# Kernel optimization log

Measured on AMD Instinct MI355X. Metric: run time of the kernel, lower is better.

## Reference

```python
import jax, jax.numpy as jnp
import numpy as np

EPS = 1e-5
K = 3

def _bn(x, g, b):
    # training-mode BatchNorm2d: batch stats over (N,H,W), biased variance
    m = jnp.mean(x, axis=(0, 2, 3), keepdims=True)
    v = jnp.var(x, axis=(0, 2, 3), keepdims=True)
    return (x - m) * jax.lax.rsqrt(v + EPS) * g[None, :, None, None] + b[None, :, None, None]

def _gelu(x):
    return jax.nn.gelu(x, approximate=False)

def _dyn_dw(x, aw1, ab1, aw2, ab2):
    # dynamic depthwise conv: per-sample k^2 softmax weights shared over channels
    b, c, h, w = x.shape
    gap = jnp.mean(x, axis=(2, 3))                              # (b,c)
    h1 = jax.nn.relu(jnp.einsum('oc,bc->bo', aw1, gap) + ab1)   # (b,c//8)
    kw = jax.nn.softmax(jnp.einsum('oc,bc->bo', aw2, h1) + ab2, axis=1)  # (b,k^2)
    xp = jnp.pad(x, ((0, 0), (0, 0), (1, 1), (1, 1)))
    out = jnp.zeros_like(x)
    idx = 0
    for i in range(K):
        for j in range(K):
            out = out + kw[:, idx, None, None, None] * xp[:, :, i:i + h, j:j + w]
            idx += 1
    return out

def _channel_att(x, w1, w2):
    avg = jnp.mean(x, axis=(2, 3))        # (b,C)
    mx = jnp.max(x, axis=(2, 3))          # (b,C)
    def fc(v):
        return jnp.einsum('oc,bc->bo', w2, jax.nn.relu(jnp.einsum('oc,bc->bo', w1, v)))
    s = jax.nn.sigmoid(fc(avg) + fc(mx))  # (b,C)
    return s[:, :, None, None] * x

def _forward(x, w1, b1, g1, be1, aw1, ab1, aw2, ab2, g2, be2,
             ca_w1, ca_w2, pw, pb, g3, be3, sw, sb):
    b, n, d = x.shape
    h = w = int(np.sqrt(n))
    residual = x
    xi = jnp.transpose(x.reshape(b, h, w, d), (0, 3, 1, 2))       # (b,d,h,w)
    # pw_expand: 1x1 conv -> GELU -> BN
    y = jnp.einsum('oc,bchw->bohw', w1, xi) + b1[None, :, None, None]
    y = _bn(_gelu(y), g1, be1)                                    # (b,4d,h,w)
    # dw_conv: dynamic depthwise -> GELU -> BN -> channel attention
    y = _dyn_dw(y, aw1, ab1, aw2, ab2)
    y = _bn(_gelu(y), g2, be2)
    y = _channel_att(y, ca_w1, ca_w2)
    # spatial attention
    avg_o = jnp.mean(y, axis=1, keepdims=True)
    max_o = jnp.max(y, axis=1, keepdims=True)
    sp_in = jnp.concatenate([avg_o, max_o], axis=1)               # (b,2,h,w)
    sp = jax.lax.conv_general_dilated(sp_in, sw, (1, 1), ((3, 3), (3, 3)),
                                      dimension_numbers=('NCHW', 'OIHW', 'NCHW'))
    sp = jax.nn.sigmoid(sp + sb[None, :, None, None])
    y = y * sp
    # pw_project: 1x1 conv -> BN
    y = jnp.einsum('oc,bchw->bohw', pw, y) + pb[None, :, None, None]
    y = _bn(y, g3, be3)
    y = jnp.transpose(y, (0, 2, 3, 1)).reshape(b, n, d)
    return residual + y

def setup_inputs() -> dict:
    key = jax.random.key(0)
    ks = jax.random.split(key, 16)
    d, C = 256, 1024
    def rn(k, shape, fan):
        return jax.random.normal(k, shape, jnp.float32) * np.float32(np.sqrt(2.0 / fan))
    return {
        'x': jax.random.normal(ks[0], (8, 1024, d), jnp.float32),
        'w1': rn(ks[1], (C, d), d), 'b1': jnp.zeros((C,), jnp.float32),
        'g1': jnp.ones((C,), jnp.float32), 'be1': jnp.zeros((C,), jnp.float32),
        'aw1': rn(ks[2], (C // 8, C), C), 'ab1': jnp.zeros((C // 8,), jnp.float32),
        'aw2': rn(ks[3], (K * K, C // 8), C // 8), 'ab2': jnp.zeros((K * K,), jnp.float32),
        'g2': jnp.ones((C,), jnp.float32), 'be2': jnp.zeros((C,), jnp.float32),
        'ca_w1': rn(ks[4], (C // 16, C), C), 'ca_w2': rn(ks[5], (C, C // 16), C // 16),
        'pw': rn(ks[6], (d, C), C), 'pb': jnp.zeros((d,), jnp.float32),
        'g3': jnp.ones((d,), jnp.float32), 'be3': jnp.zeros((d,), jnp.float32),
        'sw': rn(ks[7], (1, 2, 7, 7), 2 * 49), 'sb': jnp.zeros((1,), jnp.float32),
    }

def reference(x, w1, b1, g1, be1, aw1, ab1, aw2, ab2, g2, be2,
              ca_w1, ca_w2, pw, pb, g3, be3, sw, sb):
    return _forward(x, w1, b1, g1, be1, aw1, ab1, aw2, ab2, g2, be2,
                    ca_w1, ca_w2, pw, pb, g3, be3, sw, sb)
```

## Files before the change

### kernel.cpp

```cpp
#include <hip/hip_runtime.h>
#include <math.h>

constexpr int B = 8;
constexpr int D = 256;
constexpr int C = 1024;
constexpr int H = 32, W = 32;
constexpr int P = H * W;
constexpr int M = B * P;
constexpr float EPS = 1e-5f;

typedef unsigned short u16;
typedef unsigned int u32;
typedef __attribute__((ext_vector_type(8))) short short8;
typedef __attribute__((ext_vector_type(4))) float floatx4;

constexpr size_t WS_CHSUM1 = 0;
constexpr size_t WS_CHSQ1  = 1024;
constexpr size_t WS_GAPSUM = 2048;
constexpr size_t WS_CHSUM3 = 10240;
constexpr size_t WS_CHSQ3  = 10496;
constexpr size_t WS_CHSUM2 = 10752;
constexpr size_t WS_CHSQ2  = 11776;
constexpr size_t WS_BSUM2  = 12800;
constexpr size_t WS_UMAX2  = 20992;
constexpr size_t WS_UMAXN2 = 29184;
constexpr size_t WS_ACC_COUNT = 37376;
constexpr size_t WS_SCALE1 = 37376;
constexpr size_t WS_SHIFT1 = 38400;
constexpr size_t WS_KW     = 39424;
constexpr size_t WS_SCALE2 = 39680;
constexpr size_t WS_SHIFT2 = 40704;
constexpr size_t WS_SATT   = 41728;
constexpr size_t WS_AVGO   = 49920;
constexpr size_t WS_MAXO   = 58112;
constexpr size_t WS_SP     = 66304;
constexpr size_t WS_PRE    = 74496;
constexpr size_t WS_T1B    = 2171648;
constexpr size_t WS_T2B    = 6365952;
constexpr size_t WS_XB     = 10560256;
constexpr size_t WS_W1B    = 11608832;
constexpr size_t WS_PWB    = 11739904;
constexpr size_t WS_YB     = 11870976;

__device__ __forceinline__ float gelu_exact(float v) {
    return 0.5f * v * (1.0f + erff(v * 0.70710678118654752440f));
}

__device__ __forceinline__ u16 f2bf(float f) {
    u32 u = __float_as_uint(f);
    u += 0x7fff + ((u >> 16) & 1);
    return (u16)(u >> 16);
}

__device__ __forceinline__ float bf2f(u16 v) {
    return __uint_as_float(((u32)v) << 16);
}

__device__ __forceinline__ u32 fkey(float f) {
    u32 u = __float_as_uint(f);
    return (u & 0x80000000u) ? ~u : (u | 0x80000000u);
}
__device__ __forceinline__ float fkeyinv(u32 k) {
    return __uint_as_float((k & 0x80000000u) ? (k ^ 0x80000000u) : ~k);
}

__global__ __launch_bounds__(256) void cvt_all_kernel(const float* __restrict__ x,
                                                      const float* __restrict__ w1,
                                                      const float* __restrict__ pw,
                                                      u16* __restrict__ xb,
                                                      u16* __restrict__ w1b,
                                                      u16* __restrict__ pwb,
                                                      float* __restrict__ acc_zero) {
    const int i = blockIdx.x * 256 + threadIdx.x;
    if (i < (int)WS_ACC_COUNT) acc_zero[i] = 0.f;
    const float* src;
    u16* dst;
    int off;
    if (i < 524288)      { src = x;  dst = xb;  off = i; }
    else if (i < 589824) { src = w1; dst = w1b; off = i - 524288; }
    else                 { src = pw; dst = pwb; off = i - 589824; }
    const float4 v = *(const float4*)(src + (size_t)off * 4);
    uint2 o;
    o.x = ((u32)f2bf(v.x)) | ((u32)f2bf(v.y) << 16);
    o.y = ((u32)f2bf(v.z)) | ((u32)f2bf(v.w) << 16);
    *(uint2*)(dst + (size_t)off * 4) = o;
}

template<int KD, int EPI, int NS, int MB, int NB>
__global__ __launch_bounds__(256) void mfma_gemm_kernel(
    const u16* __restrict__ A,
    const u16* __restrict__ Bw,
    const float* __restrict__ bias,
    const float* __restrict__ rowscale,
    void* __restrict__ outv,
    float* __restrict__ csum,
    float* __restrict__ csq,
    float* __restrict__ gsum)
{
    constexpr int MI = MB / 32;
    constexpr int NJ = NB / 32;
    constexpr int ASZ = MB * 32;
    constexpr int BSZ = NB * 32;
    extern __shared__ u16 smem[];
    u16* As0 = smem;
    u16* As1 = smem + ASZ;
    u16* Bs0 = smem + 2 * ASZ;
    u16* Bs1 = smem + 2 * ASZ + BSZ;
    const int t = threadIdx.x;
    const int lane = t & 63;
    const int row0 = blockIdx.y * MB;
    const int col0 = blockIdx.x * NB;
    const int wv = t >> 6;
    const int wrow = (wv >> 1) * (MB / 2);
    const int wcol = (wv & 1) * (NB / 2);
    const int lm = lane & 15;
    const int lk8 = (lane >> 4) * 8;
    const int srow = t >> 2;
    const int scol = (t & 3) * 8;
    const u16* gA0 = A + (size_t)(row0 + srow) * KD + scol;
    const u16* gA1 = A + (size_t)(row0 + 64 + srow) * KD + scol;
    const u16* gB0 = Bw + (size_t)(col0 + srow) * KD + scol;
    const floatx4 zero = {0.f, 0.f, 0.f, 0.f};
    floatx4 acc[MI][NJ];
#pragma unroll
    for (int i = 0; i < MI; ++i)
#pragma unroll
        for (int j = 0; j < NJ; ++j) acc[i][j] = zero;

    for (int k0 = 0; k0 < KD; k0 += 64) {
        __builtin_amdgcn_global_load_lds(
            (const __attribute__((address_space(1))) void*)(gA0 + k0),
            (__attribute__((address_space(3))) void*)(As0 + t * 8), 16, 0, 0);
        if (MB == 128)
            __builtin_amdgcn_global_load_lds(
                (const __attribute__((address_space(1))) void*)(gA1 + k0),
                (__attribute__((address_space(3))) void*)(As0 + 2048 + t * 8), 16, 0, 0);
        __builtin_amdgcn_global_load_lds(
            (const __attribute__((address_space(1))) void*)(gB0 + k0),
            (__attribute__((address_space(3))) void*)(Bs0 + t * 8), 16, 0, 0);
        __builtin_amdgcn_global_load_lds(
            (const __attribute__((address_space(1))) void*)(gA0 + k0 + 32),
            (__attribute__((address_space(3))) void*)(As1 + t * 8), 16, 0, 0);
        if (MB == 128)
            __builtin_amdgcn_global_load_lds(
                (const __attribute__((address_space(1))) void*)(gA1 + k0 + 32),
                (__attribute__((address_space(3))) void*)(As1 + 2048 + t * 8), 16, 0, 0);
        __builtin_amdgcn_global_load_lds(
            (const __attribute__((address_space(1))) void*)(gB0 + k0 + 32),
            (__attribute__((address_space(3))) void*)(Bs1 + t * 8), 16, 0, 0);
        __syncthreads();
#pragma unroll
        for (int buf = 0; buf < 2; ++buf) {
            const u16* As = buf ? As1 : As0;
            const u16* Bs = buf ? Bs1 : Bs0;
            short8 af[MI], bf[NJ];
#pragma unroll
            for (int i = 0; i < MI; ++i)
                af[i] = *(const short8*)(As + (wrow + i * 16 + lm) * 32 + lk8);
#pragma unroll
            for (int j = 0; j < NJ; ++j)
                bf[j] = *(const short8*)(Bs + (wcol + j * 16 + lm) * 32 + lk8);
#pragma unroll
            for (int i = 0; i < MI; ++i)
#pragma unroll
                for (int j = 0; j < NJ; ++j)
                    acc[i][j] = __builtin_amdgcn_mfma_f32_16x16x32_bf16(af[i], bf[j], acc[i][j], 0, 0, 0);
        }
        __syncthreads();
    }

    float colsum[NJ], colsq[NJ];
#pragma unroll
    for (int j = 0; j < NJ; ++j) { colsum[j] = 0.f; colsq[j] = 0.f; }

    if (EPI == 0) {
        u16* Cs = smem;
#pragma unroll
        for (int i = 0; i < MI; ++i) {
#pragma unroll
            for (int r = 0; r < 4; ++r) {
                const int lrow = wrow + i * 16 + (lane >> 4) * 4 + r;
#pragma unroll
                for (int j = 0; j < NJ; ++j) {
                    const int lcol = wcol + j * 16 + lm;
                    const float tv = gelu_exact(acc[i][j][r] + bias[col0 + lcol]);
                    Cs[lrow * NB + lcol] = f2bf(tv);
                    colsum[j] += tv;
                    colsq[j] = fmaf(tv, tv, colsq[j]);
                }
            }
        }
        __syncthreads();
        const int rr = t >> 1;
        const int hh = (t & 1) * 32;
        u16* outp = (u16*)outv + (size_t)(row0 + rr) * NS + col0 + hh;
#pragma unroll
        for (int k = 0; k < 4; ++k) {
            *(uint4*)(outp + k * 8) = *(const uint4*)(Cs + rr * NB + hh + k * 8);
        }
    } else {
        float* Cs = (float*)smem;
#pragma unroll
        for (int i = 0; i < MI; ++i) {
#pragma unroll
            for (int r = 0; r < 4; ++r) {
                const int lrow = wrow + i * 16 + (lane >> 4) * 4 + r;
                const float rs = rowscale[row0 + lrow];
#pragma unroll
                for (int j = 0; j < NJ; ++j) {
                    const int lcol = wcol + j * 16 + lm;
                    const float tv = rs * acc[i][j][r] + bias[col0 + lcol];
                    Cs[lrow * NB + lcol] = tv;
                    colsum[j] += tv;
                    colsq[j] = fmaf(tv, tv, colsq[j]);
                }
            }
        }
        __syncthreads();
        const int rr = t >> 2;
        const int hh = (t & 3) * 16;
        float* outp = (float*)outv + (size_t)(row0 + rr) * NS + col0 + hh;
#pragma unroll
        for (int k = 0; k < 4; ++k)
            *(float4*)(outp + k * 4) = *(const float4*)(Cs + rr * NB + hh + k * 4);
    }

    const int bb = (blockIdx.y * MB) >> 10;
#pragma unroll
    for (int j = 0; j < NJ; ++j) {
        float s = colsum[j];
        float q = colsq[j];
        s += __shfl_xor(s, 16); s += __shfl_xor(s, 32);
        q += __shfl_xor(q, 16); q += __shfl_xor(q, 32);
        if (lane < 16) {
            const int c = col0 + wcol + j * 16 + lm;
            atomicAdd(&csum[c], s);
            atomicAdd(&csq[c], q);
            if (EPI == 0) atomicAdd(&gsum[bb * NS + c], s);
        }
    }
}

__global__ __launch_bounds__(1024) void dynmlp_kernel(const float* __restrict__ chsum1,
                                                      const float* __restrict__ chsq1,
                                                      const float* __restrict__ gapsum,
                                                      const float* __restrict__ g1,
                                                      const float* __restrict__ be1,
                                                      const float* __restrict__ aw1,
                                                      const float* __restrict__ ab1,
                                                      const float* __restrict__ aw2,
                                                      const float* __restrict__ ab2,
                                                      float* __restrict__ scale1,
                                                      float* __restrict__ shift1,
                                                      float* __restrict__ kw) {
    const int b = blockIdx.x;
    const int t = threadIdx.x;
    const int wave = t >> 6, lane = t & 63;
    __shared__ float g[1024];
    __shared__ float h1[128];
    __shared__ float logits[12];
    {
        const float m = chsum1[t] * (1.0f / (float)M);
        const float var = chsq1[t] * (1.0f / (float)M) - m * m;
        const float rstd = rsqrtf(var + EPS);
        const float sc = rstd * g1[t];
        const float sh = be1[t] - m * sc;
        if (b == 0) { scale1[t] = sc; shift1[t] = sh; }
        g[t] = gapsum[b * C + t] * (1.0f / (float)P) * sc + sh;
    }
    __syncthreads();
#pragma unroll
    for (int k = 0; k < 8; ++k) {
        const int u = wave * 8 + k;
        const float4* wr = (const float4*)(aw1 + (size_t)u * C);
        float s = 0.f;
#pragma unroll
        for (int ch = 0; ch < 4; ++ch) {
            const float4 wv = wr[lane + 64 * ch];
            const float4 sv = *(const float4*)(g + 4 * lane + 256 * ch);
            s += wv.x * sv.x + wv.y * sv.y + wv.z * sv.z + wv.w * sv.w;
        }
#pragma unroll
        for (int off = 1; off < 64; off <<= 1) s += __shfl_xor(s, off);
        if (lane == 0) h1[u] = fmaxf(s + ab1[u], 0.f);
    }
    __syncthreads();
    if (wave < 9) {
        float s = aw2[wave * 128 + lane] * h1[lane]
                + aw2[wave * 128 + 64 + lane] * h1[64 + lane];
#pragma unroll
        for (int off = 1; off < 64; off <<= 1) s += __shfl_xor(s, off);
        if (lane == 0) logits[wave] = s + ab2[wave];
    }
    __syncthreads();
    if (t == 0) {
        float mx = logits[0];
        for (int i = 1; i < 9; ++i) mx = fmaxf(mx, logits[i]);
        float e[9], den = 0.f;
        for (int i = 0; i < 9; ++i) { e[i] = expf(logits[i] - mx); den += e[i]; }
        const float inv = 1.0f / den;
        for (int i = 0; i < 9; ++i) kw[b * 9 + i] = e[i] * inv;
    }
}

__global__ __launch_bounds__(256) void dwconv_kernel(const u16* __restrict__ t1b,
                                                     const float* __restrict__ scale1,
                                                     const float* __restrict__ shift1,
                                                     const float* __restrict__ kw,
                                                     u16* __restrict__ t2b,
                                                     float* __restrict__ chsum2,
                                                     float* __restrict__ chsq2,
                                                     float* __restrict__ bsum2,
                                                     u32* __restrict__ umax2,
                                                     u32* __restrict__ umaxn2) {
    __shared__ u16 rows[3 * 32 * 256];
    const int bh = blockIdx.y;
    const int b = bh >> 5;
    const int h = bh & 31;
    const int cq = blockIdx.x;
    const int t = threadIdx.x;

    const u16* gbase = t1b + (size_t)b * P * C + cq * 256;
#pragma unroll
    for (int i = 0; i < 12; ++i) {
        const int lin = i * 256 + t;
        const int chunk = lin >> 5;
        const int r = chunk >> 5;
        const int w = chunk & 31;
        const int off8 = (lin & 31) * 8;
        const int hr = h + r - 1;
        uint4 v = {0u, 0u, 0u, 0u};
        if (hr >= 0 && hr < H)
            v = *(const uint4*)(gbase + (size_t)(hr * W + w) * C + off8);
        *(uint4*)(&rows[chunk * 256 + off8]) = v;
    }
    __syncthreads();

    const int c = t;
    const int gc = cq * 256 + c;
    float k[9];
#pragma unroll
    for (int i = 0; i < 9; ++i) k[i] = kw[b * 9 + i];
    const float sc = scale1[gc];
    const float sh = shift1[gc];
    const bool rok[3] = { h > 0, true, h < H - 1 };

    float s = 0.f, q = 0.f, mx = -INFINITY, mn = INFINITY;
    for (int w = 0; w < W; ++w) {
        float acc = 0.f;
#pragma unroll
        for (int ri = 0; ri < 3; ++ri) {
            if (!rok[ri]) continue;
            const u16* rp = rows + (ri * 32) * 256 + c;
            if (w > 0)
                acc = fmaf(k[ri * 3 + 0], fmaf(bf2f(rp[(w - 1) * 256]), sc, sh), acc);
            acc = fmaf(k[ri * 3 + 1], fmaf(bf2f(rp[w * 256]), sc, sh), acc);
            if (w < W - 1)
                acc = fmaf(k[ri * 3 + 2], fmaf(bf2f(rp[(w + 1) * 256]), sc, sh), acc);
        }
        const float y = gelu_exact(acc);
        t2b[((size_t)b * P + h * W + w) * C + gc] = f2bf(y);
        s += y;
        q = fmaf(y, y, q);
        mx = fmaxf(mx, y);
        mn = fminf(mn, y);
    }
    atomicAdd(&chsum2[gc], s);
    atomicAdd(&chsq2[gc], q);
    atomicAdd(&bsum2[b * C + gc], s);
    atomicMax(&umax2[b * C + gc], fkey(mx));
    atomicMax(&umaxn2[b * C + gc], fkey(-mn));
}

__global__ __launch_bounds__(1024) void chatt_kernel(const float* __restrict__ chsum2,
                                                     const float* __restrict__ chsq2,
                                                     const float* __restrict__ bsum2,
                                                     const u32* __restrict__ umax2,
                                                     const u32* __restrict__ umaxn2,
                                                     const float* __restrict__ g2,
                                                     const float* __restrict__ be2,
                                                     const float* __restrict__ caw1,
                                                     const float* __restrict__ caw2,
                                                     float* __restrict__ scale2,
                                                     float* __restrict__ shift2,
                                                     float* __restrict__ s_att) {
    const int b = blockIdx.x;
    const int t = threadIdx.x;
    const int wave = t >> 6, lane = t & 63;
    __shared__ float la[1024], lx[1024], ha[64], hm[64];
    {
        const float m = chsum2[t] * (1.0f / (float)M);
        const float var = chsq2[t] * (1.0f / (float)M) - m * m;
        const float rstd = rsqrtf(var + EPS);
        const float sc = rstd * g2[t];
        const float sh = be2[t] - m * sc;
        if (b == 0) { scale2[t] = sc; shift2[t] = sh; }
        la[t] = bsum2[b * C + t] * (1.0f / (float)P) * sc + sh;
        const float mx = fkeyinv(umax2[b * C + t]);
        const float mn = -fkeyinv(umaxn2[b * C + t]);
        lx[t] = (sc >= 0.f ? mx : mn) * sc + sh;
    }
    __syncthreads();
#pragma unroll
    for (int k = 0; k < 8; ++k) {
        const int u = wave * 8 + k;
        const int row = u & 63;
        const float* src = (u < 64) ? la : lx;
        const float4* wr = (const float4*)(caw1 + (size_t)row * C);
        float s = 0.f;
#pragma unroll
        for (int ch = 0; ch < 4; ++ch) {
            const float4 wv = wr[lane + 64 * ch];
            const float4 sv = *(const float4*)(src + 4 * lane + 256 * ch);
            s += wv.x * sv.x + wv.y * sv.y + wv.z * sv.z + wv.w * sv.w;
        }
#pragma unroll
        for (int off = 1; off < 64; off <<= 1) s += __shfl_xor(s, off);
        if (lane == 0) {
            s = fmaxf(s, 0.f);
            if (u < 64) ha[row] = s; else hm[row] = s;
        }
    }
    __syncthreads();
    {
        const float4* w2 = (const float4*)(caw2 + (size_t)t * 64);
        float s = 0.f;
#pragma unroll
        for (int j = 0; j < 16; ++j) {
            const float4 wv = w2[j];
            s += wv.x * (ha[j * 4 + 0] + hm[j * 4 + 0]);
            s += wv.y * (ha[j * 4 + 1] + hm[j * 4 + 1]);
            s += wv.z * (ha[j * 4 + 2] + hm[j * 4 + 2]);
            s += wv.w * (ha[j * 4 + 3] + hm[j * 4 + 3]);
        }
        s_att[b * C + t] = 1.0f / (1.0f + expf(-s));
    }
}

__global__ __launch_bounds__(256) void yq_kernel(const u16* __restrict__ t2b,
                                                 const float* __restrict__ scale2,
                                                 const float* __restrict__ shift2,
                                                 const float* __restrict__ s_att,
                                                 u16* __restrict__ yb,
                                                 float* __restrict__ avg_o,
                                                 float* __restrict__ max_o) {
    const int row = blockIdx.x;
    const int b = row >> 10;
    const int t = threadIdx.x;
    const int c0 = t * 4;
    const uint2 vv = *(const uint2*)(t2b + (size_t)row * C + c0);
    const float v0 = bf2f((u16)(vv.x & 0xffff));
    const float v1 = bf2f((u16)(vv.x >> 16));
    const float v2 = bf2f((u16)(vv.y & 0xffff));
    const float v3 = bf2f((u16)(vv.y >> 16));
    const float4 sc = *(const float4*)(scale2 + c0);
    const float4 sh = *(const float4*)(shift2 + c0);
    const float4 sa = *(const float4*)(s_att + (size_t)b * C + c0);
    const float y0 = fmaf(v0, sc.x, sh.x) * sa.x;
    const float y1 = fmaf(v1, sc.y, sh.y) * sa.y;
    const float y2 = fmaf(v2, sc.z, sh.z) * sa.z;
    const float y3 = fmaf(v3, sc.w, sh.w) * sa.w;
    uint2 o;
    o.x = ((u32)f2bf(y0)) | ((u32)f2bf(y1) << 16);
    o.y = ((u32)f2bf(y2)) | ((u32)f2bf(y3) << 16);
    *(uint2*)(yb + (size_t)row * C + c0) = o;
    float s = (y0 + y1) + (y2 + y3);
    float mx = fmaxf(fmaxf(y0, y1), fmaxf(y2, y3));
#pragma unroll
    for (int off = 32; off > 0; off >>= 1) {
        s += __shfl_down(s, off);
        mx = fmaxf(mx, __shfl_down(mx, off));
    }
    __shared__ float ss[4], sm[4];
    const int wave = t >> 6, lane = t & 63;
    if (lane == 0) { ss[wave] = s; sm[wave] = mx; }
    __syncthreads();
    if (t == 0) {
        const float S = ss[0] + ss[1] + ss[2] + ss[3];
        const float Mx = fmaxf(fmaxf(sm[0], sm[1]), fmaxf(sm[2], sm[3]));
        avg_o[row] = S * (1.0f / (float)C);
        max_o[row] = Mx;
    }
}

__global__ __launch_bounds__(1024) void spconv_kernel(const float* __restrict__ avg_o,
                                                      const float* __restrict__ max_o,
                                                      const float* __restrict__ sw,
                                                      const float* __restrict__ sb,
                                                      float* __restrict__ sp) {
    const int b = blockIdx.x;
    const int t = threadIdx.x;
    __shared__ float pa[P], pm[P], wsh[98];
    pa[t] = avg_o[b * P + t];
    pm[t] = max_o[b * P + t];
    if (t < 98) wsh[t] = sw[t];
    const float sbv = sb[0];
    __syncthreads();
    const int h = t >> 5, w = t & 31;
    float acc = sbv;
#pragma unroll
    for (int i = 0; i < 7; ++i) {
        const int hh = h + i - 3;
        if (hh < 0 || hh >= H) continue;
#pragma unroll
        for (int j = 0; j < 7; ++j) {
            const int ww = w + j - 3;
            if (ww < 0 || ww >= W) continue;
            const int pidx = hh * W + ww;
            acc = fmaf(wsh[i * 7 + j], pa[pidx], acc);
            acc = fmaf(wsh[49 + i * 7 + j], pm[pidx], acc);
        }
    }
    sp[b * P + t] = 1.0f / (1.0f + expf(-acc));
}

__global__ __launch_bounds__(256) void final_kernel(const float* __restrict__ x,
                                                    const float* __restrict__ pre,
                                                    const float* __restrict__ chsum3,
                                                    const float* __restrict__ chsq3,
                                                    const float* __restrict__ g3,
                                                    const float* __restrict__ be3,
                                                    float* __restrict__ out) {
    __shared__ float lsc[256], lsh[256];
    const int t = threadIdx.x;
    {
        const float m = chsum3[t] * (1.0f / (float)M);
        const float var = chsq3[t] * (1.0f / (float)M) - m * m;
        const float rstd = rsqrtf(var + EPS);
        const float sc = rstd * g3[t];
        lsc[t] = sc;
        lsh[t] = be3[t] - m * sc;
    }
    __syncthreads();
    const int i = blockIdx.x * 256 + t;
    const int e = i * 4;
    const int d = e & 255;
    const float4 xv = *(const float4*)(x + e);
    const float4 pv = *(const float4*)(pre + e);
    const float4 sc = *(const float4*)(lsc + d);
    const float4 sh = *(const float4*)(lsh + d);
    float4 o;
    o.x = xv.x + fmaf(pv.x, sc.x, sh.x);
    o.y = xv.y + fmaf(pv.y, sc.y, sh.y);
    o.z = xv.z + fmaf(pv.z, sc.z, sh.z);
    o.w = xv.w + fmaf(pv.w, sc.w, sh.w);
    *(float4*)(out + e) = o;
}

extern "C" void kernel_launch(void* const* d_in, const int* in_sizes, int n_in,
                              void* d_out, int out_size, void* d_ws, size_t ws_size,
                              hipStream_t stream) {
    const float* x    = (const float*)d_in[0];
    const float* w1   = (const float*)d_in[1];
    const float* b1   = (const float*)d_in[2];
    const float* g1   = (const float*)d_in[3];
    const float* be1  = (const float*)d_in[4];
    const float* aw1  = (const float*)d_in[5];
    const float* ab1  = (const float*)d_in[6];
    const float* aw2  = (const float*)d_in[7];
    const float* ab2  = (const float*)d_in[8];
    const float* g2   = (const float*)d_in[9];
    const float* be2  = (const float*)d_in[10];
    const float* caw1 = (const float*)d_in[11];
    const float* caw2 = (const float*)d_in[12];
    const float* pw   = (const float*)d_in[13];
    const float* pb   = (const float*)d_in[14];
    const float* g3   = (const float*)d_in[15];
    const float* be3  = (const float*)d_in[16];
    const float* sw   = (const float*)d_in[17];
    const float* sb   = (const float*)d_in[18];
    float* out = (float*)d_out;
    float* ws = (float*)d_ws;

    float* chsum1  = ws + WS_CHSUM1;
    float* chsq1   = ws + WS_CHSQ1;
    float* gapsum  = ws + WS_GAPSUM;
    float* chsum3  = ws + WS_CHSUM3;
    float* chsq3   = ws + WS_CHSQ3;
    float* chsum2  = ws + WS_CHSUM2;
    float* chsq2   = ws + WS_CHSQ2;
    float* bsum2   = ws + WS_BSUM2;
    u32*   umax2   = (u32*)(ws + WS_UMAX2);
    u32*   umaxn2  = (u32*)(ws + WS_UMAXN2);
    float* scale1  = ws + WS_SCALE1;
    float* shift1  = ws + WS_SHIFT1;
    float* kw      = ws + WS_KW;
    float* scale2  = ws + WS_SCALE2;
    float* shift2  = ws + WS_SHIFT2;
    float* s_att   = ws + WS_SATT;
    float* avg_o   = ws + WS_AVGO;
    float* max_o   = ws + WS_MAXO;
    float* sp      = ws + WS_SP;
    float* pre     = ws + WS_PRE;
    u16* t1b = (u16*)(ws + WS_T1B);
    u16* t2b = (u16*)(ws + WS_T2B);
    u16* xb  = (u16*)(ws + WS_XB);
    u16* w1b = (u16*)(ws + WS_W1B);
    u16* pwb = (u16*)(ws + WS_PWB);
    u16* yb  = (u16*)(ws + WS_YB);

    cvt_all_kernel<<<dim3(2560), 256, 0, stream>>>(x, w1, pw, xb, w1b, pwb, ws);
    mfma_gemm_kernel<256, 0, C, 128, 64><<<dim3(C / 64, M / 128), 256, 24576, stream>>>(
        xb, w1b, b1, nullptr, t1b, chsum1, chsq1, gapsum);
    dynmlp_kernel<<<dim3(B), 1024, 0, stream>>>(chsum1, chsq1, gapsum, g1, be1,
                                                aw1, ab1, aw2, ab2, scale1, shift1, kw);
    dwconv_kernel<<<dim3(4, B * H), 256, 0, stream>>>(t1b, scale1, shift1, kw, t2b,
                                                      chsum2, chsq2, bsum2, umax2, umaxn2);
    chatt_kernel<<<dim3(B), 1024, 0, stream>>>(chsum2, chsq2, bsum2, umax2, umaxn2,
                                               g2, be2, caw1, caw2, scale2, shift2, s_att);
    yq_kernel<<<dim3(M), 256, 0, stream>>>(t2b, scale2, shift2, s_att, yb, avg_o, max_o);
    spconv_kernel<<<dim3(B), 1024, 0, stream>>>(avg_o, max_o, sw, sb, sp);
    mfma_gemm_kernel<1024, 1, D, 64, 64><<<dim3(D / 64, M / 64), 256, 16384, stream>>>(
        yb, pwb, pb, sp, pre, chsum3, chsq3, nullptr);
    final_kernel<<<dim3((M * D / 4) / 256), 256, 0, stream>>>(x, pre, chsum3, chsq3, g3, be3, out);
}
```

Before: 213.0 us.

## Double-buffer GEMM K loop, enlarge tile, swizzle blocks, slide dwconv window

The GEMM main loop now prefetches the next 64-wide K chunk into a second LDS buffer while computing on the current one, so global-to-LDS loads overlap MFMA work. The first GEMM moves to a 128x128 tile, and both GEMMs remap block indices so that neighbouring workgroups are spread across 8 groups, which may help cache or XCD locality. The depthwise conv replaces its per-pixel 3x3 reloads with a sliding register window and folds the border rows in by zeroing scale and shift. The cost is more LDS per block (64KB for the first GEMM), which lowers occupancy.

After: 207.4 us. 2.6% less time.

```diff
diff --git a/kernel.cpp b/kernel.cpp
--- a/kernel.cpp
+++ b/kernel.cpp
@@ -64,6 +64,10 @@
     return __uint_as_float((k & 0x80000000u) ? (k ^ 0x80000000u) : ~k);
 }
 
+#define GLOAD(SRC, DST) __builtin_amdgcn_global_load_lds( \
+    (const __attribute__((address_space(1))) void*)(SRC), \
+    (__attribute__((address_space(3))) void*)(DST), 16, 0, 0)
+
 __global__ __launch_bounds__(256) void cvt_all_kernel(const float* __restrict__ x,
                                                       const float* __restrict__ w1,
                                                       const float* __restrict__ pw,
@@ -99,17 +103,26 @@
 {
     constexpr int MI = MB / 32;
     constexpr int NJ = NB / 32;
-    constexpr int ASZ = MB * 32;
-    constexpr int BSZ = NB * 32;
+    constexpr int ABUF = MB * 64;
+    constexpr int BBUF = NB * 64;
+    constexpr int GX = NS / NB;
+    constexpr int NWG = (M / MB) * GX;
+    constexpr int CPX = NWG / 8;
     extern __shared__ u16 smem[];
-    u16* As0 = smem;
-    u16* As1 = smem + ASZ;
-    u16* Bs0 = smem + 2 * ASZ;
-    u16* Bs1 = smem + 2 * ASZ + BSZ;
+    u16* Ab0 = smem;
+    u16* Ab1 = smem + ABUF;
+    u16* Bb0 = smem + 2 * ABUF;
+    u16* Bb1 = smem + 2 * ABUF + BBUF;
     const int t = threadIdx.x;
     const int lane = t & 63;
-    const int row0 = blockIdx.y * MB;
-    const int col0 = blockIdx.x * NB;
+
+    const int lin = blockIdx.y * GX + blockIdx.x;
+    const int swz = (lin & 7) * CPX + (lin >> 3);
+    const int bx = swz % GX;
+    const int by = swz / GX;
+    const int row0 = by * MB;
+    const int col0 = bx * NB;
+
     const int wv = t >> 6;
     const int wrow = (wv >> 1) * (MB / 2);
     const int wcol = (wv & 1) * (NB / 2);
@@ -120,6 +133,8 @@
     const u16* gA0 = A + (size_t)(row0 + srow) * KD + scol;
     const u16* gA1 = A + (size_t)(row0 + 64 + srow) * KD + scol;
     const u16* gB0 = Bw + (size_t)(col0 + srow) * KD + scol;
+    const u16* gB1 = Bw + (size_t)(col0 + 64 + srow) * KD + scol;
+
     const floatx4 zero = {0.f, 0.f, 0.f, 0.f};
     floatx4 acc[MI][NJ];
 #pragma unroll
@@ -127,46 +142,46 @@
 #pragma unroll
         for (int j = 0; j < NJ; ++j) acc[i][j] = zero;
 
-    for (int k0 = 0; k0 < KD; k0 += 64) {
-        __builtin_amdgcn_global_load_lds(
-            (const __attribute__((address_space(1))) void*)(gA0 + k0),
-            (__attribute__((address_space(3))) void*)(As0 + t * 8), 16, 0, 0);
-        if (MB == 128)
-            __builtin_amdgcn_global_load_lds(
-                (const __attribute__((address_space(1))) void*)(gA1 + k0),
-                (__attribute__((address_space(3))) void*)(As0 + 2048 + t * 8), 16, 0, 0);
-        __builtin_amdgcn_global_load_lds(
-            (const __attribute__((address_space(1))) void*)(gB0 + k0),
-            (__attribute__((address_space(3))) void*)(Bs0 + t * 8), 16, 0, 0);
-        __builtin_amdgcn_global_load_lds(
-            (const __attribute__((address_space(1))) void*)(gA0 + k0 + 32),
-            (__attribute__((address_space(3))) void*)(As1 + t * 8), 16, 0, 0);
-        if (MB == 128)
-            __builtin_amdgcn_global_load_lds(
-                (const __attribute__((address_space(1))) void*)(gA1 + k0 + 32),
-                (__attribute__((address_space(3))) void*)(As1 + 2048 + t * 8), 16, 0, 0);
-        __builtin_amdgcn_global_load_lds(
-            (const __attribute__((address_space(1))) void*)(gB0 + k0 + 32),
-            (__attribute__((address_space(3))) void*)(Bs1 + t * 8), 16, 0, 0);
-        __syncthreads();
-#pragma unroll
-        for (int buf = 0; buf < 2; ++buf) {
-            const u16* As = buf ? As1 : As0;
-            const u16* Bs = buf ? Bs1 : Bs0;
+    auto stage = [&](u16* As, u16* Bs, int k0) {
+#pragma unroll
+        for (int s2 = 0; s2 < 2; ++s2) {
+            const int kk = k0 + s2 * 32;
+            u16* Asub = As + s2 * (MB * 32);
+            u16* Bsub = Bs + s2 * (NB * 32);
+            GLOAD(gA0 + kk, Asub + t * 8);
+            if constexpr (MB == 128) GLOAD(gA1 + kk, Asub + 2048 + t * 8);
+            GLOAD(gB0 + kk, Bsub + t * 8);
+            if constexpr (NB == 128) GLOAD(gB1 + kk, Bsub + 2048 + t * 8);
+        }
+    };
+    auto compute = [&](const u16* As, const u16* Bs) {
+#pragma unroll
+        for (int s2 = 0; s2 < 2; ++s2) {
+            const u16* Asub = As + s2 * (MB * 32);
+            const u16* Bsub = Bs + s2 * (NB * 32);
             short8 af[MI], bf[NJ];
 #pragma unroll
             for (int i = 0; i < MI; ++i)
-                af[i] = *(const short8*)(As + (wrow + i * 16 + lm) * 32 + lk8);
+                af[i] = *(const short8*)(Asub + (wrow + i * 16 + lm) * 32 + lk8);
 #pragma unroll
             for (int j = 0; j < NJ; ++j)
-                bf[j] = *(const short8*)(Bs + (wcol + j * 16 + lm) * 32 + lk8);
+                bf[j] = *(const short8*)(Bsub + (wcol + j * 16 + lm) * 32 + lk8);
 #pragma unroll
             for (int i = 0; i < MI; ++i)
 #pragma unroll
                 for (int j = 0; j < NJ; ++j)
                     acc[i][j] = __builtin_amdgcn_mfma_f32_16x16x32_bf16(af[i], bf[j], acc[i][j], 0, 0, 0);
         }
+    };
+
+    stage(Ab0, Bb0, 0);
+    __syncthreads();
+    int cur = 0;
+    for (int k0 = 0; k0 < KD; k0 += 64) {
+        if (k0 + 64 < KD) stage(cur ? Ab0 : Ab1, cur ? Bb0 : Bb1, k0 + 64);
+        compute(cur ? Ab1 : Ab0, cur ? Bb1 : Bb0);
         __syncthreads();
+        cur ^= 1;
     }
 
     float colsum[NJ], colsq[NJ];
@@ -191,12 +206,15 @@
             }
         }
         __syncthreads();
-        const int rr = t >> 1;
-        const int hh = (t & 1) * 32;
-        u16* outp = (u16*)outv + (size_t)(row0 + rr) * NS + col0 + hh;
-#pragma unroll
-        for (int k = 0; k < 4; ++k) {
-            *(uint4*)(outp + k * 8) = *(const uint4*)(Cs + rr * NB + hh + k * 8);
+        constexpr int TPR = NB / 8;
+        constexpr int RPP = 256 / TPR;
+        u16* outp = (u16*)outv;
+#pragma unroll
+        for (int p = 0; p < MB / RPP; ++p) {
+            const int r = p * RPP + t / TPR;
+            const int cc = (t % TPR) * 8;
+            *(uint4*)(outp + (size_t)(row0 + r) * NS + col0 + cc) =
+                *(const uint4*)(Cs + r * NB + cc);
         }
     } else {
         float* Cs = (float*)smem;
@@ -217,15 +235,19 @@
             }
         }
         __syncthreads();
-        const int rr = t >> 2;
-        const int hh = (t & 3) * 16;
-        float* outp = (float*)outv + (size_t)(row0 + rr) * NS + col0 + hh;
-#pragma unroll
-        for (int k = 0; k < 4; ++k)
-            *(float4*)(outp + k * 4) = *(const float4*)(Cs + rr * NB + hh + k * 4);
-    }
-
-    const int bb = (blockIdx.y * MB) >> 10;
+        constexpr int TPR = NB / 4;
+        constexpr int RPP = 256 / TPR;
+        float* outp = (float*)outv;
+#pragma unroll
+        for (int p = 0; p < MB / RPP; ++p) {
+            const int r = p * RPP + t / TPR;
+            const int cc = (t % TPR) * 4;
+            *(float4*)(outp + (size_t)(row0 + r) * NS + col0 + cc) =
+                *(const float4*)(Cs + r * NB + cc);
+        }
+    }
+
+    const int bb = (by * MB) >> 10;
 #pragma unroll
     for (int j = 0; j < NJ; ++j) {
         float s = colsum[j];
@@ -314,20 +336,22 @@
                                                      u32* __restrict__ umax2,
                                                      u32* __restrict__ umaxn2) {
     __shared__ u16 rows[3 * 32 * 256];
-    const int bh = blockIdx.y;
+    const int lin = blockIdx.y * 4 + blockIdx.x;
+    const int swz = (lin & 7) * 128 + (lin >> 3);
+    const int cq = swz & 3;
+    const int bh = swz >> 2;
     const int b = bh >> 5;
     const int h = bh & 31;
-    const int cq = blockIdx.x;
     const int t = threadIdx.x;
 
     const u16* gbase = t1b + (size_t)b * P * C + cq * 256;
 #pragma unroll
     for (int i = 0; i < 12; ++i) {
-        const int lin = i * 256 + t;
-        const int chunk = lin >> 5;
+        const int lin2 = i * 256 + t;
+        const int chunk = lin2 >> 5;
         const int r = chunk >> 5;
         const int w = chunk & 31;
-        const int off8 = (lin & 31) * 8;
+        const int off8 = (lin2 & 31) * 8;
         const int hr = h + r - 1;
         uint4 v = {0u, 0u, 0u, 0u};
         if (hr >= 0 && hr < H)
@@ -338,33 +362,54 @@
 
     const int c = t;
     const int gc = cq * 256 + c;
-    float k[9];
-#pragma unroll
-    for (int i = 0; i < 9; ++i) k[i] = kw[b * 9 + i];
+    float kk[9];
+#pragma unroll
+    for (int i = 0; i < 9; ++i) kk[i] = kw[b * 9 + i];
     const float sc = scale1[gc];
     const float sh = shift1[gc];
-    const bool rok[3] = { h > 0, true, h < H - 1 };
+    float scm[3], shm[3];
+    scm[0] = (h > 0)     ? sc : 0.f;  shm[0] = (h > 0)     ? sh : 0.f;
+    scm[1] = sc;                      shm[1] = sh;
+    scm[2] = (h < H - 1) ? sc : 0.f;  shm[2] = (h < H - 1) ? sh : 0.f;
+
+    const u16* rp0 = rows + c;
+#define DWVAL(ri, w) fmaf(bf2f(rp0[((ri) * 32 + (w)) * 256]), scm[ri], shm[ri])
+
+    float vm0 = 0.f, vm1 = 0.f, vm2 = 0.f;
+    float vc0 = DWVAL(0, 0), vc1 = DWVAL(1, 0), vc2 = DWVAL(2, 0);
+    float vp0 = DWVAL(0, 1), vp1 = DWVAL(1, 1), vp2 = DWVAL(2, 1);
 
     float s = 0.f, q = 0.f, mx = -INFINITY, mn = INFINITY;
+    u16* orow = t2b + ((size_t)b * P + h * W) * C + gc;
     for (int w = 0; w < W; ++w) {
-        float acc = 0.f;
-#pragma unroll
-        for (int ri = 0; ri < 3; ++ri) {
-            if (!rok[ri]) continue;
-            const u16* rp = rows + (ri * 32) * 256 + c;
-            if (w > 0)
-                acc = fmaf(k[ri * 3 + 0], fmaf(bf2f(rp[(w - 1) * 256]), sc, sh), acc);
-            acc = fmaf(k[ri * 3 + 1], fmaf(bf2f(rp[w * 256]), sc, sh), acc);
-            if (w < W - 1)
-                acc = fmaf(k[ri * 3 + 2], fmaf(bf2f(rp[(w + 1) * 256]), sc, sh), acc);
-        }
+        float acc;
+        acc = kk[0] * vm0;
+        acc = fmaf(kk[1], vc0, acc);
+        acc = fmaf(kk[2], vp0, acc);
+        acc = fmaf(kk[3], vm1, acc);
+        acc = fmaf(kk[4], vc1, acc);
+        acc = fmaf(kk[5], vp1, acc);
+        acc = fmaf(kk[6], vm2, acc);
+        acc = fmaf(kk[7], vc2, acc);
+        acc = fmaf(kk[8], vp2, acc);
         const float y = gelu_exact(acc);
-        t2b[((size_t)b * P + h * W + w) * C + gc] = f2bf(y);
+        orow[(size_t)w * C] = f2bf(y);
         s += y;
         q = fmaf(y, y, q);
         mx = fmaxf(mx, y);
         mn = fminf(mn, y);
-    }
+        vm0 = vc0; vc0 = vp0;
+        vm1 = vc1; vc1 = vp1;
+        vm2 = vc2; vc2 = vp2;
+        if (w + 2 < W) {
+            vp0 = DWVAL(0, w + 2);
+            vp1 = DWVAL(1, w + 2);
+            vp2 = DWVAL(2, w + 2);
+        } else {
+            vp0 = 0.f; vp1 = 0.f; vp2 = 0.f;
+        }
+    }
+#undef DWVAL
     atomicAdd(&chsum2[gc], s);
     atomicAdd(&chsq2[gc], q);
     atomicAdd(&bsum2[b * C + gc], s);
@@ -600,7 +645,7 @@
     u16* yb  = (u16*)(ws + WS_YB);
 
     cvt_all_kernel<<<dim3(2560), 256, 0, stream>>>(x, w1, pw, xb, w1b, pwb, ws);
-    mfma_gemm_kernel<256, 0, C, 128, 64><<<dim3(C / 64, M / 128), 256, 24576, stream>>>(
+    mfma_gemm_kernel<256, 0, C, 128, 128><<<dim3(C / 128, M / 128), 256, 65536, stream>>>(
         xb, w1b, b1, nullptr, t1b, chsum1, chsq1, gapsum);
     dynmlp_kernel<<<dim3(B), 1024, 0, stream>>>(chsum1, chsq1, gapsum, g1, be1,
                                                 aw1, ab1, aw2, ab2, scale1, shift1, kw);
@@ -610,7 +655,7 @@
                                                g2, be2, caw1, caw2, scale2, shift2, s_att);
     yq_kernel<<<dim3(M), 256, 0, stream>>>(t2b, scale2, shift2, s_att, yb, avg_o, max_o);
     spconv_kernel<<<dim3(B), 1024, 0, stream>>>(avg_o, max_o, sw, sb, sp);
-    mfma_gemm_kernel<1024, 1, D, 64, 64><<<dim3(D / 64, M / 64), 256, 16384, stream>>>(
+    mfma_gemm_kernel<1024, 1, D, 64, 64><<<dim3(D / 64, M / 64), 256, 32768, stream>>>(
         yb, pwb, pb, sp, pre, chsum3, chsq3, nullptr);
     final_kernel<<<dim3((M * D / 4) / 256), 256, 0, stream>>>(x, pre, chsum3, chsq3, g3, be3, out);
 }
```
